# Performance work log

Measured on AMD Instinct MI355X. Metric: run time of the kernel, lower is better.

The kernel has to match this reference:

```python
import jax, jax.numpy as jnp
import numpy as np

N_NODES = 1_000_000
N_EDGES = 16_000_000


def setup_inputs() -> dict:
    key = jax.random.key(0)
    k_feat, k_norm, k_src, k_dst, k_w1, k_w2 = jax.random.split(key, 6)
    feat = jax.random.normal(k_feat, (N_NODES, 1), dtype=jnp.float32)
    norm = jax.random.uniform(k_norm, (N_NODES, 1), dtype=jnp.float32)
    src = jax.random.randint(k_src, (N_EDGES,), 0, N_NODES, dtype=jnp.int64 if jax.config.read('jax_enable_x64') else jnp.int32)
    dst = jax.random.randint(k_dst, (N_EDGES,), 0, N_NODES, dtype=jnp.int64 if jax.config.read('jax_enable_x64') else jnp.int32)
    # GCNLayer1: in_feats=1 -> out_feats=3; GCNLayer2: 3 -> 1 (hardcoded in GCNProtein)
    W1 = jax.random.normal(k_w1, (1, 3), dtype=jnp.float32) * (1.0 / np.sqrt(1.0))
    b1 = jnp.zeros((3,), dtype=jnp.float32)
    W2 = jax.random.normal(k_w2, (3, 1), dtype=jnp.float32) * (1.0 / np.sqrt(3.0))
    b2 = jnp.zeros((1,), dtype=jnp.float32)
    return {"feat": feat, "norm": norm, "src": src, "dst": dst,
            "W1": W1, "b1": b1, "W2": W2, "b2": b2}


def gcn_layer(src, dst, x, norm, W, b):
    # symmetric-normalized GCN message passing (DGL GraphConv semantics):
    # h = norm * x ; h = sum_{(u->v) in E} h[u] scattered to v ; h = norm * h ; h = h @ W + b ; relu
    h = x * norm                                   # [N, F]
    msgs = jnp.take(h, src, axis=0)                # [E, F] gather (irregular)
    agg = jax.ops.segment_sum(msgs, dst, num_segments=x.shape[0])  # [N, F] scatter-add
    h = agg * norm                                 # [N, F]
    h = h @ W + b                                  # tiny GEMM: F_in -> F_out
    return jax.nn.relu(h)


def reference(feat, norm, src, dst, W1, b1, W2, b2):
    h = gcn_layer(src, dst, feat, norm, W1, b1)    # [N, 3]
    h = gcn_layer(src, dst, h, norm, W2, b2)       # [N, 1]
    return h
```

## Files before the change

kernel.cpp:

```cpp
#include <hip/hip_runtime.h>

#define BSHIFT 11
#define BSZ (1 << BSHIFT)
#define NBIN_BLOCKS 1024
#define PB 512
#define BATCH 8192


__global__ void k1b(const float* __restrict__ feat, const float* __restrict__ norm,
                    float* __restrict__ g1, int n) {
    int stride = gridDim.x * blockDim.x;
    for (int i = blockIdx.x * blockDim.x + threadIdx.x; i < n; i += stride)
        g1[i] = feat[i] * norm[i];
}

__global__ void k1_prep(const float* __restrict__ feat, const float* __restrict__ norm,
                        float* __restrict__ g1, float* __restrict__ agg1,
                        float* __restrict__ agg2, int n) {
    int stride = gridDim.x * blockDim.x;
    for (int i = blockIdx.x * blockDim.x + threadIdx.x; i < n; i += stride) {
        g1[i] = feat[i] * norm[i];
        agg1[i] = 0.0f;
        agg2[i] = 0.0f;
    }
}

__global__ void k3_mid(const float* __restrict__ agg1, const float* __restrict__ norm,
                       const float* __restrict__ W1, const float* __restrict__ b1,
                       const float* __restrict__ W2, float* __restrict__ t, int n) {
    float w10 = W1[0], w11 = W1[1], w12 = W1[2];
    float b10 = b1[0], b11 = b1[1], b12 = b1[2];
    float w20 = W2[0], w21 = W2[1], w22 = W2[2];
    int stride = gridDim.x * blockDim.x;
    for (int i = blockIdx.x * blockDim.x + threadIdx.x; i < n; i += stride) {
        float nv = norm[i];
        float s = agg1[i] * nv;
        float h0 = fmaxf(fmaf(s, w10, b10), 0.0f);
        float h1 = fmaxf(fmaf(s, w11, b11), 0.0f);
        float h2 = fmaxf(fmaf(s, w12, b12), 0.0f);
        t[i] = nv * (h0 * w20 + h1 * w21 + h2 * w22);
    }
}

__global__ void k5_out(const float* __restrict__ agg2, const float* __restrict__ norm,
                       const float* __restrict__ b2, float* __restrict__ out, int n) {
    float b = b2[0];
    int stride = gridDim.x * blockDim.x;
    for (int i = blockIdx.x * blockDim.x + threadIdx.x; i < n; i += stride)
        out[i] = fmaxf(agg2[i] * norm[i] + b, 0.0f);
}


__global__ void k_hist(const int* __restrict__ dst, int nE, int NB, int chunk,
                       int* __restrict__ counts) {
    extern __shared__ int lhist[];
    int t = threadIdx.x;
    for (int b = t; b < NB; b += blockDim.x) lhist[b] = 0;
    __syncthreads();
    int lo = blockIdx.x * chunk;
    int hi = min(lo + chunk, nE);
    int n4 = (hi - lo) >> 2;
    const int4* d4 = (const int4*)(dst + lo);
    for (int i = t; i < n4; i += blockDim.x) {
        int4 v = d4[i];
        atomicAdd(&lhist[v.x >> BSHIFT], 1);
        atomicAdd(&lhist[v.y >> BSHIFT], 1);
        atomicAdd(&lhist[v.z >> BSHIFT], 1);
        atomicAdd(&lhist[v.w >> BSHIFT], 1);
    }
    for (int i = lo + (n4 << 2) + t; i < hi; i += blockDim.x)
        atomicAdd(&lhist[dst[i] >> BSHIFT], 1);
    __syncthreads();
    for (int b = t; b < NB; b += blockDim.x)
        counts[(size_t)b * NBIN_BLOCKS + blockIdx.x] = lhist[b];
}

__global__ void k_bucketscan(const int* __restrict__ counts,
                             int* __restrict__ chunkpre, int* __restrict__ tot) {
    __shared__ int ssum[256];
    int b = blockIdx.x;
    int t = threadIdx.x;
    const int4* in4 = (const int4*)(counts + (size_t)b * NBIN_BLOCKS);
    int4 v = in4[t];
    int mysum = v.x + v.y + v.z + v.w;
    ssum[t] = mysum;
    __syncthreads();
    for (int ofs = 1; ofs < 256; ofs <<= 1) {
        int add = (t >= ofs) ? ssum[t - ofs] : 0;
        __syncthreads();
        ssum[t] += add;
        __syncthreads();
    }
    int excl = ssum[t] - mysum;
    int4 o;
    o.x = excl;
    o.y = excl + v.x;
    o.z = o.y + v.y;
    o.w = o.z + v.z;
    ((int4*)(chunkpre + (size_t)b * NBIN_BLOCKS))[t] = o;
    if (t == 255) tot[b] = ssum[255];
}

__global__ void k_exscan(const int* __restrict__ tot, int NB, int* __restrict__ base) {
    __shared__ int s[1024];
    int t = threadIdx.x;
    if (NB < 1024) {
        int v = (t < NB) ? tot[t] : 0;
        s[t] = v;
        __syncthreads();
        for (int ofs = 1; ofs < 1024; ofs <<= 1) {
            int add = (t >= ofs) ? s[t - ofs] : 0;
            __syncthreads();
            s[t] += add;
            __syncthreads();
        }
        if (t < NB) base[t] = s[t] - v;
        if (t == NB) base[NB] = s[NB - 1];
    } else if (t == 0) {
        int run = 0;
        for (int b = 0; b < NB; ++b) { base[b] = run; run += tot[b]; }
        base[NB] = run;
    }
}

__global__ void __launch_bounds__(PB)
k_place2(const int* __restrict__ src, const int* __restrict__ dst,
         int nE, int NB, int chunk,
         const int* __restrict__ chunkpre, const int* __restrict__ base,
         unsigned int* __restrict__ bpack) {
    __shared__ unsigned int spack[BATCH];
    __shared__ unsigned short sbkt[BATCH];
    __shared__ int lcur[512];
    __shared__ int loff[513];
    __shared__ int gcur[512];
    __shared__ int ssc[512];
    int t = threadIdx.x;
    int blk = blockIdx.x;

    for (int b = t; b < NB; b += PB)
        gcur[b] = base[b] + chunkpre[(size_t)b * NBIN_BLOCKS + blk];

    int lo = blk * chunk;
    int hi = min(lo + chunk, nE);
    for (int bs = lo; bs < hi; bs += BATCH) {
        int be = min(bs + BATCH, hi);
        int cnt = be - bs;
        lcur[t] = 0;
        __syncthreads();
        int n4 = cnt >> 2;
        const int4* d4 = (const int4*)(dst + bs);
        for (int i = t; i < n4; i += PB) {
            int4 v = d4[i];
            atomicAdd(&lcur[v.x >> BSHIFT], 1);
            atomicAdd(&lcur[v.y >> BSHIFT], 1);
            atomicAdd(&lcur[v.z >> BSHIFT], 1);
            atomicAdd(&lcur[v.w >> BSHIFT], 1);
        }
        for (int i = bs + (n4 << 2) + t; i < be; i += PB)
            atomicAdd(&lcur[dst[i] >> BSHIFT], 1);
        __syncthreads();
        int v = lcur[t];
        ssc[t] = v;
        __syncthreads();
        for (int ofs = 1; ofs < 512; ofs <<= 1) {
            int add = (t >= ofs) ? ssc[t - ofs] : 0;
            __syncthreads();
            ssc[t] += add;
            __syncthreads();
        }
        int excl = ssc[t] - v;
        loff[t] = excl;
        lcur[t] = excl;
        if (t == 511) loff[512] = ssc[511];
        __syncthreads();
        const int4* s4 = (const int4*)(src + bs);
        for (int i = t; i < n4; i += PB) {
            int4 dv = d4[i];
            int4 sv = s4[i];
            int b0 = dv.x >> BSHIFT, p0 = atomicAdd(&lcur[b0], 1);
            spack[p0] = ((unsigned int)sv.x << BSHIFT) | (unsigned int)(dv.x & (BSZ - 1));
            sbkt[p0] = (unsigned short)b0;
            int b1 = dv.y >> BSHIFT, p1 = atomicAdd(&lcur[b1], 1);
            spack[p1] = ((unsigned int)sv.y << BSHIFT) | (unsigned int)(dv.y & (BSZ - 1));
            sbkt[p1] = (unsigned short)b1;
            int b2 = dv.z >> BSHIFT, p2 = atomicAdd(&lcur[b2], 1);
            spack[p2] = ((unsigned int)sv.z << BSHIFT) | (unsigned int)(dv.z & (BSZ - 1));
            sbkt[p2] = (unsigned short)b2;
            int b3 = dv.w >> BSHIFT, p3 = atomicAdd(&lcur[b3], 1);
            spack[p3] = ((unsigned int)sv.w << BSHIFT) | (unsigned int)(dv.w & (BSZ - 1));
            sbkt[p3] = (unsigned short)b3;
        }
        for (int i = bs + (n4 << 2) + t; i < be; i += PB) {
            int d = dst[i];
            int b = d >> BSHIFT;
            int pos = atomicAdd(&lcur[b], 1);
            spack[pos] = ((unsigned int)src[i] << BSHIFT) | (unsigned int)(d & (BSZ - 1));
            sbkt[pos] = (unsigned short)b;
        }
        __syncthreads();
        for (int j = t; j < cnt; j += PB) {
            int b = sbkt[j];
            bpack[gcur[b] + (j - loff[b])] = spack[j];
        }
        __syncthreads();
        for (int b = t; b < NB; b += PB)
            gcur[b] += loff[b + 1] - loff[b];
        __syncthreads();
    }
}

__global__ void k_acc1(const unsigned int* __restrict__ bpack,
                       const int* __restrict__ base,
                       const float* __restrict__ val, const float* __restrict__ norm,
                       const float* __restrict__ W1, const float* __restrict__ b1,
                       const float* __restrict__ W2,
                       float* __restrict__ t, int nN) {
    __shared__ float acc[BSZ];
    for (int j = threadIdx.x; j < BSZ; j += blockDim.x) acc[j] = 0.0f;
    __syncthreads();
    int b = blockIdx.x;
    int lo = base[b], hi = base[b + 1];
    int head = min((4 - (lo & 3)) & 3, hi - lo);
    for (int i = lo + (int)threadIdx.x; i < lo + head; i += blockDim.x) {
        unsigned int w = bpack[i];
        atomicAdd(&acc[w & (BSZ - 1)], val[w >> BSHIFT]);
    }
    int lo4 = lo + head;
    int n4 = (hi - lo4) >> 2;
    const uint4* p4 = (const uint4*)(bpack + lo4);
    for (int i = threadIdx.x; i < n4; i += blockDim.x) {
        uint4 w = p4[i];
        atomicAdd(&acc[w.x & (BSZ - 1)], val[w.x >> BSHIFT]);
        atomicAdd(&acc[w.y & (BSZ - 1)], val[w.y >> BSHIFT]);
        atomicAdd(&acc[w.z & (BSZ - 1)], val[w.z >> BSHIFT]);
        atomicAdd(&acc[w.w & (BSZ - 1)], val[w.w >> BSHIFT]);
    }
    for (int i = lo4 + (n4 << 2) + (int)threadIdx.x; i < hi; i += blockDim.x) {
        unsigned int w = bpack[i];
        atomicAdd(&acc[w & (BSZ - 1)], val[w >> BSHIFT]);
    }
    __syncthreads();
    float w10 = W1[0], w11 = W1[1], w12 = W1[2];
    float b10 = b1[0], b11 = b1[1], b12 = b1[2];
    float w20 = W2[0], w21 = W2[1], w22 = W2[2];
    int node0 = b << BSHIFT;
    for (int j = threadIdx.x; j < BSZ && node0 + j < nN; j += blockDim.x) {
        float nv = norm[node0 + j];
        float s = acc[j] * nv;
        float h0 = fmaxf(fmaf(s, w10, b10), 0.0f);
        float h1 = fmaxf(fmaf(s, w11, b11), 0.0f);
        float h2 = fmaxf(fmaf(s, w12, b12), 0.0f);
        t[node0 + j] = nv * (h0 * w20 + h1 * w21 + h2 * w22);
    }
}

__global__ void k_acc2(const unsigned int* __restrict__ bpack,
                       const int* __restrict__ base,
                       const float* __restrict__ val, const float* __restrict__ norm,
                       const float* __restrict__ b2,
                       float* __restrict__ out, int nN) {
    __shared__ float acc[BSZ];
    for (int j = threadIdx.x; j < BSZ; j += blockDim.x) acc[j] = 0.0f;
    __syncthreads();
    int b = blockIdx.x;
    int lo = base[b], hi = base[b + 1];
    int head = min((4 - (lo & 3)) & 3, hi - lo);
    for (int i = lo + (int)threadIdx.x; i < lo + head; i += blockDim.x) {
        unsigned int w = bpack[i];
        atomicAdd(&acc[w & (BSZ - 1)], val[w >> BSHIFT]);
    }
    int lo4 = lo + head;
    int n4 = (hi - lo4) >> 2;
    const uint4* p4 = (const uint4*)(bpack + lo4);
    for (int i = threadIdx.x; i < n4; i += blockDim.x) {
        uint4 w = p4[i];
        atomicAdd(&acc[w.x & (BSZ - 1)], val[w.x >> BSHIFT]);
        atomicAdd(&acc[w.y & (BSZ - 1)], val[w.y >> BSHIFT]);
        atomicAdd(&acc[w.z & (BSZ - 1)], val[w.z >> BSHIFT]);
        atomicAdd(&acc[w.w & (BSZ - 1)], val[w.w >> BSHIFT]);
    }
    for (int i = lo4 + (n4 << 2) + (int)threadIdx.x; i < hi; i += blockDim.x) {
        unsigned int w = bpack[i];
        atomicAdd(&acc[w & (BSZ - 1)], val[w >> BSHIFT]);
    }
    __syncthreads();
    float bb = b2[0];
    int node0 = b << BSHIFT;
    for (int j = threadIdx.x; j < BSZ && node0 + j < nN; j += blockDim.x)
        out[node0 + j] = fmaxf(acc[j] * norm[node0 + j] + bb, 0.0f);
}

__global__ void k_edge_scatter(const int* __restrict__ src, const int* __restrict__ dst,
                               const float* __restrict__ val, float* __restrict__ agg,
                               int nE) {
    int stride = gridDim.x * blockDim.x;
    for (int e = blockIdx.x * blockDim.x + threadIdx.x; e < nE; e += stride)
        atomicAdd(&agg[dst[e]], val[src[e]]);
}

static inline size_t align256(size_t x) { return (x + 255) & ~(size_t)255; }

extern "C" void kernel_launch(void* const* d_in, const int* in_sizes, int n_in,
                              void* d_out, int out_size, void* d_ws, size_t ws_size,
                              hipStream_t stream) {
    const float* feat = (const float*)d_in[0];
    const float* norm = (const float*)d_in[1];
    const int*   src  = (const int*)d_in[2];
    const int*   dst  = (const int*)d_in[3];
    const float* W1   = (const float*)d_in[4];
    const float* b1   = (const float*)d_in[5];
    const float* W2   = (const float*)d_in[6];
    const float* b2   = (const float*)d_in[7];
    float* out = (float*)d_out;

    int nN = in_sizes[0];
    int nE = in_sizes[2];
    int NB = (nN + BSZ - 1) >> BSHIFT;

    char* p = (char*)d_ws;
    size_t off = 0;
    float* g1   = (float*)(p + off); off = align256(off + (size_t)nN * 4);
    float* agg1 = (float*)(p + off); off = align256(off + (size_t)nN * 4);
    float* agg2 = (float*)(p + off); off = align256(off + (size_t)nN * 4);
    int* base     = (int*)(p + off); off = align256(off + (size_t)(NB + 1) * 4);
    int* tot      = (int*)(p + off); off = align256(off + (size_t)NB * 4);
    int* counts   = (int*)(p + off); off = align256(off + (size_t)NB * NBIN_BLOCKS * 4);
    int* chunkpre = (int*)(p + off); off = align256(off + (size_t)NB * NBIN_BLOCKS * 4);
    unsigned int* bpack = (unsigned int*)(p + off); off = align256(off + (size_t)nE * 4);
    size_t need = off;

    const int BLK = 256;
    int nodeBlocks = (nN + BLK - 1) / BLK;
    if (nodeBlocks > 2048) nodeBlocks = 2048;

    bool packed_ok = ((size_t)nN <= ((size_t)1 << (32 - BSHIFT))) && (NB <= 512);
    if (ws_size >= need && packed_ok) {
        int chunk = (nE + NBIN_BLOCKS - 1) / NBIN_BLOCKS;
        chunk = (chunk + 3) & ~3;
        size_t ldsNB = (size_t)NB * 4;

        k1b<<<nodeBlocks, BLK, 0, stream>>>(feat, norm, g1, nN);
        k_hist<<<NBIN_BLOCKS, 256, ldsNB, stream>>>(dst, nE, NB, chunk, counts);
        k_bucketscan<<<NB, 256, 0, stream>>>(counts, chunkpre, tot);
        k_exscan<<<1, 1024, 0, stream>>>(tot, NB, base);
        k_place2<<<NBIN_BLOCKS, PB, 0, stream>>>(src, dst, nE, NB, chunk,
                                                 chunkpre, base, bpack);
        k_acc1<<<NB, 512, 0, stream>>>(bpack, base, g1, norm, W1, b1, W2, agg1, nN);
        k_acc2<<<NB, 512, 0, stream>>>(bpack, base, agg1, norm, b2, out, nN);
    } else {
        int edgeBlocks = 2048;
        k1_prep<<<nodeBlocks, BLK, 0, stream>>>(feat, norm, g1, agg1, agg2, nN);
        k_edge_scatter<<<edgeBlocks, BLK, 0, stream>>>(src, dst, g1, agg1, nE);
        k3_mid<<<nodeBlocks, BLK, 0, stream>>>(agg1, norm, W1, b1, W2, g1, nN);
        k_edge_scatter<<<edgeBlocks, BLK, 0, stream>>>(src, dst, g1, agg2, nE);
        k5_out<<<nodeBlocks, BLK, 0, stream>>>(agg2, norm, b2, out, nN);
    }
}
```

Before: 264.6 us.

## Halve bucket width to 1024 nodes and double-issue gathers in accumulation

```diff
diff --git a/kernel.cpp b/kernel.cpp
--- a/kernel.cpp
+++ b/kernel.cpp
@@ -1,7 +1,8 @@
 #include <hip/hip_runtime.h>
 
-#define BSHIFT 11
+#define BSHIFT 10
 #define BSZ (1 << BSHIFT)
+#define NBMAX 1024
 #define NBIN_BLOCKS 1024
 #define PB 512
 #define BATCH 8192
@@ -130,10 +131,10 @@
          unsigned int* __restrict__ bpack) {
     __shared__ unsigned int spack[BATCH];
     __shared__ unsigned short sbkt[BATCH];
-    __shared__ int lcur[512];
-    __shared__ int loff[513];
-    __shared__ int gcur[512];
-    __shared__ int ssc[512];
+    __shared__ int lcur[NBMAX];
+    __shared__ int loff[NBMAX + 1];
+    __shared__ int gcur[NBMAX];
+    __shared__ int ssc[PB];
     int t = threadIdx.x;
     int blk = blockIdx.x;
 
@@ -145,7 +146,8 @@
     for (int bs = lo; bs < hi; bs += BATCH) {
         int be = min(bs + BATCH, hi);
         int cnt = be - bs;
-        lcur[t] = 0;
+        lcur[2 * t] = 0;
+        lcur[2 * t + 1] = 0;
         __syncthreads();
         int n4 = cnt >> 2;
         const int4* d4 = (const int4*)(dst + bs);
@@ -159,19 +161,23 @@
         for (int i = bs + (n4 << 2) + t; i < be; i += PB)
             atomicAdd(&lcur[dst[i] >> BSHIFT], 1);
         __syncthreads();
-        int v = lcur[t];
-        ssc[t] = v;
-        __syncthreads();
-        for (int ofs = 1; ofs < 512; ofs <<= 1) {
+        int a = lcur[2 * t];
+        int c = lcur[2 * t + 1];
+        int s = a + c;
+        ssc[t] = s;
+        __syncthreads();
+        for (int ofs = 1; ofs < PB; ofs <<= 1) {
             int add = (t >= ofs) ? ssc[t - ofs] : 0;
             __syncthreads();
             ssc[t] += add;
             __syncthreads();
         }
-        int excl = ssc[t] - v;
-        loff[t] = excl;
-        lcur[t] = excl;
-        if (t == 511) loff[512] = ssc[511];
+        int excl = ssc[t] - s;
+        loff[2 * t] = excl;
+        loff[2 * t + 1] = excl + a;
+        lcur[2 * t] = excl;
+        lcur[2 * t + 1] = excl + a;
+        if (t == PB - 1) loff[2 * PB] = ssc[PB - 1];
         __syncthreads();
         const int4* s4 = (const int4*)(src + bs);
         for (int i = t; i < n4; i += PB) {
@@ -209,6 +215,49 @@
     }
 }
 
+__device__ __forceinline__ void acc_body(const unsigned int* __restrict__ bpack,
+                                         int lo, int hi,
+                                         const float* __restrict__ val,
+                                         float* acc) {
+    int head = min((4 - (lo & 3)) & 3, hi - lo);
+    for (int i = lo + (int)threadIdx.x; i < lo + head; i += blockDim.x) {
+        unsigned int w = bpack[i];
+        atomicAdd(&acc[w & (BSZ - 1)], val[w >> BSHIFT]);
+    }
+    int lo4 = lo + head;
+    int n4 = (hi - lo4) >> 2;
+    const uint4* p4 = (const uint4*)(bpack + lo4);
+    int i = threadIdx.x;
+    int bd = blockDim.x;
+    for (; i + bd < n4; i += 2 * bd) {
+        uint4 wa = p4[i];
+        uint4 wb = p4[i + bd];
+        float va0 = val[wa.x >> BSHIFT], va1 = val[wa.y >> BSHIFT];
+        float va2 = val[wa.z >> BSHIFT], va3 = val[wa.w >> BSHIFT];
+        float vb0 = val[wb.x >> BSHIFT], vb1 = val[wb.y >> BSHIFT];
+        float vb2 = val[wb.z >> BSHIFT], vb3 = val[wb.w >> BSHIFT];
+        atomicAdd(&acc[wa.x & (BSZ - 1)], va0);
+        atomicAdd(&acc[wa.y & (BSZ - 1)], va1);
+        atomicAdd(&acc[wa.z & (BSZ - 1)], va2);
+        atomicAdd(&acc[wa.w & (BSZ - 1)], va3);
+        atomicAdd(&acc[wb.x & (BSZ - 1)], vb0);
+        atomicAdd(&acc[wb.y & (BSZ - 1)], vb1);
+        atomicAdd(&acc[wb.z & (BSZ - 1)], vb2);
+        atomicAdd(&acc[wb.w & (BSZ - 1)], vb3);
+    }
+    for (; i < n4; i += bd) {
+        uint4 w = p4[i];
+        atomicAdd(&acc[w.x & (BSZ - 1)], val[w.x >> BSHIFT]);
+        atomicAdd(&acc[w.y & (BSZ - 1)], val[w.y >> BSHIFT]);
+        atomicAdd(&acc[w.z & (BSZ - 1)], val[w.z >> BSHIFT]);
+        atomicAdd(&acc[w.w & (BSZ - 1)], val[w.w >> BSHIFT]);
+    }
+    for (int j = lo4 + (n4 << 2) + (int)threadIdx.x; j < hi; j += blockDim.x) {
+        unsigned int w = bpack[j];
+        atomicAdd(&acc[w & (BSZ - 1)], val[w >> BSHIFT]);
+    }
+}
+
 __global__ void k_acc1(const unsigned int* __restrict__ bpack,
                        const int* __restrict__ base,
                        const float* __restrict__ val, const float* __restrict__ norm,
@@ -219,26 +268,7 @@
     for (int j = threadIdx.x; j < BSZ; j += blockDim.x) acc[j] = 0.0f;
     __syncthreads();
     int b = blockIdx.x;
-    int lo = base[b], hi = base[b + 1];
-    int head = min((4 - (lo & 3)) & 3, hi - lo);
-    for (int i = lo + (int)threadIdx.x; i < lo + head; i += blockDim.x) {
-        unsigned int w = bpack[i];
-        atomicAdd(&acc[w & (BSZ - 1)], val[w >> BSHIFT]);
-    }
-    int lo4 = lo + head;
-    int n4 = (hi - lo4) >> 2;
-    const uint4* p4 = (const uint4*)(bpack + lo4);
-    for (int i = threadIdx.x; i < n4; i += blockDim.x) {
-        uint4 w = p4[i];
-        atomicAdd(&acc[w.x & (BSZ - 1)], val[w.x >> BSHIFT]);
-        atomicAdd(&acc[w.y & (BSZ - 1)], val[w.y >> BSHIFT]);
-        atomicAdd(&acc[w.z & (BSZ - 1)], val[w.z >> BSHIFT]);
-        atomicAdd(&acc[w.w & (BSZ - 1)], val[w.w >> BSHIFT]);
-    }
-    for (int i = lo4 + (n4 << 2) + (int)threadIdx.x; i < hi; i += blockDim.x) {
-        unsigned int w = bpack[i];
-        atomicAdd(&acc[w & (BSZ - 1)], val[w >> BSHIFT]);
-    }
+    acc_body(bpack, base[b], base[b + 1], val, acc);
     __syncthreads();
     float w10 = W1[0], w11 = W1[1], w12 = W1[2];
     float b10 = b1[0], b11 = b1[1], b12 = b1[2];
@@ -263,26 +293,7 @@
     for (int j = threadIdx.x; j < BSZ; j += blockDim.x) acc[j] = 0.0f;
     __syncthreads();
     int b = blockIdx.x;
-    int lo = base[b], hi = base[b + 1];
-    int head = min((4 - (lo & 3)) & 3, hi - lo);
-    for (int i = lo + (int)threadIdx.x; i < lo + head; i += blockDim.x) {
-        unsigned int w = bpack[i];
-        atomicAdd(&acc[w & (BSZ - 1)], val[w >> BSHIFT]);
-    }
-    int lo4 = lo + head;
-    int n4 = (hi - lo4) >> 2;
-    const uint4* p4 = (const uint4*)(bpack + lo4);
-    for (int i = threadIdx.x; i < n4; i += blockDim.x) {
-        uint4 w = p4[i];
-        atomicAdd(&acc[w.x & (BSZ - 1)], val[w.x >> BSHIFT]);
-        atomicAdd(&acc[w.y & (BSZ - 1)], val[w.y >> BSHIFT]);
-        atomicAdd(&acc[w.z & (BSZ - 1)], val[w.z >> BSHIFT]);
-        atomicAdd(&acc[w.w & (BSZ - 1)], val[w.w >> BSHIFT]);
-    }
-    for (int i = lo4 + (n4 << 2) + (int)threadIdx.x; i < hi; i += blockDim.x) {
-        unsigned int w = bpack[i];
-        atomicAdd(&acc[w & (BSZ - 1)], val[w >> BSHIFT]);
-    }
+    acc_body(bpack, base[b], base[b + 1], val, acc);
     __syncthreads();
     float bb = b2[0];
     int node0 = b << BSHIFT;
@@ -321,9 +332,9 @@
     size_t off = 0;
     float* g1   = (float*)(p + off); off = align256(off + (size_t)nN * 4);
     float* agg1 = (float*)(p + off); off = align256(off + (size_t)nN * 4);
-    float* agg2 = (float*)(p + off); off = align256(off + (size_t)nN * 4);
     int* base     = (int*)(p + off); off = align256(off + (size_t)(NB + 1) * 4);
     int* tot      = (int*)(p + off); off = align256(off + (size_t)NB * 4);
+    float* agg2   = (float*)(p + off);
     int* counts   = (int*)(p + off); off = align256(off + (size_t)NB * NBIN_BLOCKS * 4);
     int* chunkpre = (int*)(p + off); off = align256(off + (size_t)NB * NBIN_BLOCKS * 4);
     unsigned int* bpack = (unsigned int*)(p + off); off = align256(off + (size_t)nE * 4);
@@ -333,7 +344,7 @@
     int nodeBlocks = (nN + BLK - 1) / BLK;
     if (nodeBlocks > 2048) nodeBlocks = 2048;
 
-    bool packed_ok = ((size_t)nN <= ((size_t)1 << (32 - BSHIFT))) && (NB <= 512);
+    bool packed_ok = ((size_t)nN <= ((size_t)1 << (32 - BSHIFT))) && (NB <= NBMAX);
     if (ws_size >= need && packed_ok) {
         int chunk = (nE + NBIN_BLOCKS - 1) / NBIN_BLOCKS;
         chunk = (chunk + 3) & ~3;
```

After: 282.7 us. 1.07x slower.
